# Kernel optimization log

Measured on AMD Instinct MI355X. Metric: run time of the kernel, lower is better.

The kernel has to match this reference:

```python
import jax, jax.numpy as jnp
import numpy as np

# Camera intrinsics (init kwargs of the torch module)
CAMERA_F = (248.0, 248.0)
CAMERA_C = (111.5, 111.5)
GRID_N = 41  # initial mesh = triangulated GRID_N x GRID_N grid


def _grid_faces(G):
    idx = np.arange(G * G).reshape(G, G)
    v00, v10 = idx[:-1, :-1], idx[1:, :-1]
    v01, v11 = idx[:-1, 1:], idx[1:, 1:]
    t1 = np.stack([v00, v10, v01], -1).reshape(-1, 3)
    t2 = np.stack([v10, v11, v01], -1).reshape(-1, 3)
    return np.concatenate([t1, t2], 0).astype(np.int32)


def setup_inputs() -> dict:
    key = jax.random.key(0)
    k1, k2, k3, k4 = jax.random.split(key, 4)
    verts = 0.25 * jax.random.normal(k4, (GRID_N * GRID_N, 3), jnp.float32)
    faces = jnp.asarray(_grid_faces(GRID_N))
    feat3 = jax.random.normal(k1, (256, 56, 56), jnp.float32)
    feat4 = jax.random.normal(k2, (512, 28, 28), jnp.float32)
    feat5 = jax.random.normal(k3, (512, 14, 14), jnp.float32)
    return {"feat3": feat3, "feat4": feat4, "feat5": feat5,
            "verts": verts, "faces": faces, "image_size": 224}


def _project(coords):
    # image_project: K @ [I | (0,0,0.8)] then perspective divide
    fx, fy = CAMERA_F
    cx, cy = CAMERA_C
    K = jnp.array([[fx, 0., cx], [0., fy, cy], [0., 0., 1.]], coords.dtype)
    E = jnp.array([[1., 0., 0., 0.], [0., 1., 0., 0.], [0., 0., 1., 0.8]], coords.dtype)
    P = K @ E  # [3,4]
    h = jnp.concatenate([coords, jnp.ones((coords.shape[0], 1), coords.dtype)], 1)
    pix = h @ P.T                      # [N,3]
    pix = pix / pix[:, 2:3]            # divide by s
    return pix[:, 0], pix[:, 1]


def _bilinear(x, y, feat, image_size):
    # feat: [C,H,W]; replicates original bilinear_interpolation math exactly
    dim = feat.shape[1]
    x = jnp.clip(x * dim / image_size, 0, dim - 1)
    y = jnp.clip(y * dim / image_size, 0, dim - 1)
    x1, x2 = jnp.floor(x), jnp.ceil(x)
    y1, y2 = jnp.floor(y), jnp.ceil(y)
    xi1, xi2 = x1.astype(jnp.int32), x2.astype(jnp.int32)
    yi1, yi2 = y1.astype(jnp.int32), y2.astype(jnp.int32)
    f11 = feat[:, xi1, yi1].T  # [N,C]
    f12 = feat[:, xi1, yi2].T
    f21 = feat[:, xi2, yi1].T
    f22 = feat[:, xi2, yi2].T
    w11 = ((x2 - x) * (y2 - y))[:, None]
    w12 = ((x2 - x) * (y - y1))[:, None]
    w21 = ((x - x1) * (y2 - y))[:, None]
    w22 = ((x - x1) * (y - y1))[:, None]
    return w11 * f11 + w12 * f12 + w21 * f21 + w22 * f22


def _pool(verts, feats, image_size):
    x, y = _project(verts)
    return jnp.concatenate([_bilinear(x, y, f, image_size) for f in feats], 1)


def _subdivide(vf, faces_np):
    # Vectorized equivalent of unpool_graph: one midpoint per unique
    # undirected edge, numbered by first occurrence in the per-face loop
    # order (edges (i1,i2),(i2,i3),(i3,i1) per face, faces in order).
    V = vf.shape[0]
    f = faces_np
    e = np.stack([f[:, [0, 1]], f[:, [1, 2]], f[:, [2, 0]]], 1).reshape(-1, 2)  # [3F,2]
    a, b = e.min(1), e.max(1)
    key = a.astype(np.int64) * np.int64(V) + b
    _, first_idx, inv = np.unique(key, return_index=True, return_inverse=True)
    order = np.argsort(first_idx)
    rank = np.empty(len(order), dtype=np.int64)
    rank[order] = np.arange(len(order))
    mid_idx = V + rank[inv]                       # new index per edge slot [3F]
    ue = e[np.sort(first_idx)]                    # unique edges, first-occurrence order
    mids = 0.5 * (vf[ue[:, 0]] + vf[ue[:, 1]])    # midpoint of (coords|features)
    new_vf = jnp.concatenate([vf, mids], 0)
    m = mid_idx.reshape(-1, 3)
    i1, i2, i3 = f[:, 0], f[:, 1], f[:, 2]
    i4, i5, i6 = m[:, 0], m[:, 1], m[:, 2]
    nf = np.stack([np.stack([i1, i4, i6], 1), np.stack([i2, i4, i5], 1),
                   np.stack([i3, i5, i6], 1), np.stack([i5, i4, i6], 1)], 1).reshape(-1, 3)
    return new_vf, nf.astype(np.int64)


def reference(feat3, feat4, feat5, verts, faces, image_size):
    feats = [feat3, feat4, feat5]
    faces_np = np.asarray(faces)
    # stage 1
    perc1 = _pool(verts, feats, image_size)                 # [V1,1280]
    f1 = jnp.concatenate([perc1, verts], 1)                 # [V1,1283]
    vf2, faces2 = _subdivide(jnp.concatenate([verts, f1], 1), faces_np)
    verts2, s2 = vf2[:, :3], vf2[:, 3:]
    # stage 2
    perc2 = _pool(verts2, feats, image_size)                # [V2,1280]
    f2 = jnp.concatenate([perc2, s2], 1)                    # [V2,2563]
    vf3, faces3 = _subdivide(jnp.concatenate([verts2, f2], 1), faces2)
    verts3, s3 = vf3[:, :3], vf3[:, 3:]
    # stage 3
    perc3 = _pool(verts3, feats, image_size)                # [V3,1280]
    return jnp.concatenate([perc3, s3], 1)                  # [V3,3843]
```

## Files before the change

kernel.cpp:

```cpp
#include <hip/hip_runtime.h>
#include <hip/hip_bf16.h>
#include <stdint.h>

#define NV1 1681
#define NF1 3200
#define NS1 (3*NF1)
#define NV2 6561
#define NF2 12800
#define NS2 (3*NF2)
#define NV3 25921
#define D1  1286
#define P1  1288
#define D2  2566
#define P2  2568
#define DOUT 3843
#define TSIZE 131072
#define TMASK (TSIZE-1)

__global__ __launch_bounds__(256) void transpose32(
    const float* __restrict__ in, float* __restrict__ outp, int R, int Cc)
{
  __shared__ float tile[32][33];
  int bx = blockIdx.x * 32;
  int by = blockIdx.y * 32;
  int tx = threadIdx.x, ty = threadIdx.y;
  for (int j = ty; j < 32; j += 8) {
    int r = by + j, c = bx + tx;
    if (r < R && c < Cc) tile[j][tx] = in[(size_t)r*Cc + c];
  }
  __syncthreads();
  for (int j = ty; j < 32; j += 8) {
    int orow = bx + j, oc = by + tx;
    if (orow < Cc && oc < R) outp[(size_t)orow*R + oc] = tile[tx][j];
  }
}

__global__ __launch_bounds__(320) void pool_t(
    const float* __restrict__ verts, int vstride, int nverts,
    const float* __restrict__ t3, const float* __restrict__ t4,
    const float* __restrict__ t5, float* __restrict__ out, int ostride)
{
  int v = blockIdx.x;
  if (v >= nverts) return;
  float X = verts[(size_t)v*vstride + 0];
  float Y = verts[(size_t)v*vstride + 1];
  float Z = verts[(size_t)v*vstride + 2];
  float p2 = Z + 0.8f;
  float px = (248.0f*X + 111.5f*Z + 89.2f) / p2;
  float py = (248.0f*Y + 111.5f*Z + 89.2f) / p2;

  int c4 = (int)threadIdx.x * 4;
  int m  = (c4 < 256) ? 0 : (c4 < 768) ? 1 : 2;
  int dim = (m == 0) ? 56 : (m == 1) ? 28 : 14;
  int C   = (m == 0) ? 256 : 512;
  int cb  = (m == 0) ? 0 : (m == 1) ? 256 : 768;
  const float* t = (m == 0) ? t3 : (m == 1) ? t4 : t5;

  float dimf = (float)dim;
  float x = fminf(fmaxf(px * dimf / 224.0f, 0.0f), dimf - 1.0f);
  float y = fminf(fmaxf(py * dimf / 224.0f, 0.0f), dimf - 1.0f);
  float x1 = floorf(x), x2 = ceilf(x);
  float y1 = floorf(y), y2 = ceilf(y);
  int xi1 = min(max((int)x1, 0), dim-1);
  int xi2 = min(max((int)x2, 0), dim-1);
  int yi1 = min(max((int)y1, 0), dim-1);
  int yi2 = min(max((int)y2, 0), dim-1);
  float w11 = (x2-x)*(y2-y), w12 = (x2-x)*(y-y1);
  float w21 = (x-x1)*(y2-y), w22 = (x-x1)*(y-y1);

  int cc = c4 - cb;
  const float4 f11 = *(const float4*)(t + (size_t)(xi1*dim + yi1)*C + cc);
  const float4 f12 = *(const float4*)(t + (size_t)(xi1*dim + yi2)*C + cc);
  const float4 f21 = *(const float4*)(t + (size_t)(xi2*dim + yi1)*C + cc);
  const float4 f22 = *(const float4*)(t + (size_t)(xi2*dim + yi2)*C + cc);

  float* o = out + (size_t)v*ostride + c4;
  o[0] = w11*f11.x + w12*f12.x + w21*f21.x + w22*f22.x;
  o[1] = w11*f11.y + w12*f12.y + w21*f21.y + w22*f22.y;
  o[2] = w11*f11.z + w12*f12.z + w21*f21.z + w22*f22.z;
  o[3] = w11*f11.w + w12*f12.w + w21*f21.w + w22*f22.w;
}

__global__ void copyverts1(const float* __restrict__ verts, float* __restrict__ vf1)
{
  int i = blockIdx.x*blockDim.x + threadIdx.x;
  if (i >= NV1*3) return;
  int r = i/3, c = i - 3*r;
  float v = verts[i];
  vf1[(size_t)r*P1 + c] = v;
  vf1[(size_t)r*P1 + 1283 + c] = v;
}

__global__ void edge_insert(const int* __restrict__ faces, int F, int V,
                            unsigned* __restrict__ tkey, int* __restrict__ tmin,
                            unsigned* __restrict__ keys)
{
  int s = blockIdx.x*blockDim.x + threadIdx.x;
  if (s >= 3*F) return;
  int f = s/3, k = s - 3*f;
  int a0 = faces[3*f + k];
  int a1 = faces[3*f + (k == 2 ? 0 : k+1)];
  int a = min(a0, a1), b = max(a0, a1);
  unsigned key = (unsigned)a * (unsigned)V + (unsigned)b;
  keys[s] = key;
  unsigned h = (key * 2654435761u) & TMASK;
  while (true) {
    unsigned old = atomicCAS(&tkey[h], 0xFFFFFFFFu, key);
    if (old == 0xFFFFFFFFu || old == key) { atomicMin(&tmin[h], s); break; }
    h = (h+1) & TMASK;
  }
}

__global__ void edge_first(const unsigned* __restrict__ keys, int S,
                           const unsigned* __restrict__ tkey, const int* __restrict__ tmin,
                           int* __restrict__ fslot)
{
  int s = blockIdx.x*blockDim.x + threadIdx.x;
  if (s >= S) return;
  unsigned key = keys[s];
  unsigned h = (key * 2654435761u) & TMASK;
  while (tkey[h] != key) h = (h+1) & TMASK;
  fslot[s] = tmin[h];
}

__global__ __launch_bounds__(1024) void scan_excl(const int* __restrict__ fslot,
                                                  int* __restrict__ ranks, int n)
{
  __shared__ int tmp[1024];
  int tid = (int)threadIdx.x;
  int npt = (n + 1023) >> 10;
  int base = tid * npt;
  int cnt = 0;
  for (int j = 0; j < npt; ++j) {
    int i = base + j;
    if (i < n && fslot[i] == i) cnt++;
  }
  tmp[tid] = cnt;
  __syncthreads();
  for (int off = 1; off < 1024; off <<= 1) {
    int t = (tid >= off) ? tmp[tid - off] : 0;
    __syncthreads();
    tmp[tid] += t;
    __syncthreads();
  }
  int run = tmp[tid] - cnt;
  for (int j = 0; j < npt; ++j) {
    int i = base + j;
    if (i < n) { ranks[i] = run; if (fslot[i] == i) run++; }
  }
}

__global__ void edge_mid(const unsigned* __restrict__ keys, const int* __restrict__ fslot,
                         const int* __restrict__ ranks, int S, int V,
                         int* __restrict__ mid, int* __restrict__ uea, int* __restrict__ ueb)
{
  int s = blockIdx.x*blockDim.x + threadIdx.x;
  if (s >= S) return;
  int fs = fslot[s];
  int r = ranks[fs];
  mid[s] = V + r;
  if (fs == s) {
    unsigned key = keys[s];
    uea[r] = (int)(key / (unsigned)V);
    ueb[r] = (int)(key % (unsigned)V);
  }
}

__global__ void new_faces(const int* __restrict__ faces, int F,
                          const int* __restrict__ mid, int* __restrict__ nf)
{
  int f = blockIdx.x*blockDim.x + threadIdx.x;
  if (f >= F) return;
  int i1 = faces[3*f], i2 = faces[3*f+1], i3 = faces[3*f+2];
  int i4 = mid[3*f], i5 = mid[3*f+1], i6 = mid[3*f+2];
  int* o = nf + 12*f;
  o[0]=i1; o[1]=i4; o[2]=i6;
  o[3]=i2; o[4]=i4; o[5]=i5;
  o[6]=i3; o[7]=i5; o[8]=i6;
  o[9]=i5; o[10]=i4; o[11]=i6;
}

__global__ __launch_bounds__(256) void subdivide4(
    const float* __restrict__ src, int P, int D, int Vold,
    const int* __restrict__ uea, const int* __restrict__ ueb,
    float* __restrict__ dstV, int dvs, float* __restrict__ dstS, int dss)
{
  int c4 = (blockIdx.x*256 + (int)threadIdx.x) * 4;
  int r = blockIdx.y;
  if (c4 >= D) return;
  float4 val;
  if (r < Vold) {
    val = *(const float4*)(src + (size_t)r*P + c4);
  } else {
    int e = r - Vold;
    int a = uea[e], b = ueb[e];
    float4 va = *(const float4*)(src + (size_t)a*P + c4);
    float4 vb = *(const float4*)(src + (size_t)b*P + c4);
    val.x = 0.5f*(va.x+vb.x); val.y = 0.5f*(va.y+vb.y);
    val.z = 0.5f*(va.z+vb.z); val.w = 0.5f*(va.w+vb.w);
  }
  float vv[4] = {val.x, val.y, val.z, val.w};
#pragma unroll
  for (int t = 0; t < 4; ++t) {
    int c = c4 + t;
    if (c < D) {
      if (c < 3) dstV[(size_t)r*dvs + c] = vv[t];
      else       dstS[(size_t)r*dss + (c-3)] = vv[t];
    }
  }
}

static inline char* bump(char*& p, size_t bytes) {
  char* r = p;
  p += (bytes + 255) & ~(size_t)255;
  return r;
}

extern "C" void kernel_launch(void* const* d_in, const int* in_sizes, int n_in,
                              void* d_out, int out_size, void* d_ws, size_t ws_size,
                              hipStream_t stream)
{
  const float* f3    = (const float*)d_in[0];
  const float* f4    = (const float*)d_in[1];
  const float* f5    = (const float*)d_in[2];
  const float* verts = (const float*)d_in[3];
  const int*   faces = (const int*)d_in[4];
  float* out = (float*)d_out;

  char* p = (char*)d_ws;
  float* t3     = (float*)bump(p, (size_t)3136*256*4);
  float* t4     = (float*)bump(p, (size_t)784*512*4);
  float* t5     = (float*)bump(p, (size_t)196*512*4);
  float* vf1    = (float*)bump(p, (size_t)NV1*P1*4);
  float* vf2    = (float*)bump(p, (size_t)NV2*P2*4);
  float* verts3 = (float*)bump(p, (size_t)NV3*3*4);
  int*   faces2 = (int*)  bump(p, (size_t)NF2*3*4);
  unsigned* key1 = (unsigned*)bump(p, (size_t)NS1*4);
  int* fslot1 = (int*)bump(p, (size_t)NS1*4);
  int* rank1  = (int*)bump(p, (size_t)NS1*4);
  int* mid1   = (int*)bump(p, (size_t)NS1*4);
  int* ue1a   = (int*)bump(p, (size_t)NS1*4);
  int* ue1b   = (int*)bump(p, (size_t)NS1*4);
  unsigned* key2 = (unsigned*)bump(p, (size_t)NS2*4);
  int* fslot2 = (int*)bump(p, (size_t)NS2*4);
  int* rank2  = (int*)bump(p, (size_t)NS2*4);
  int* mid2   = (int*)bump(p, (size_t)NS2*4);
  int* ue2a   = (int*)bump(p, (size_t)NS2*4);
  int* ue2b   = (int*)bump(p, (size_t)NS2*4);
  unsigned* tkey1 = (unsigned*)bump(p, (size_t)TSIZE*4);
  int*      tmin1 = (int*)     bump(p, (size_t)TSIZE*4);
  unsigned* tkey2 = (unsigned*)bump(p, (size_t)TSIZE*4);
  int*      tmin2 = (int*)     bump(p, (size_t)TSIZE*4);

  hipMemsetAsync(tkey1, 0xFF, (size_t)TSIZE*4, stream);
  hipMemsetAsync(tmin1, 0x7F, (size_t)TSIZE*4, stream);
  hipMemsetAsync(tkey2, 0xFF, (size_t)TSIZE*4, stream);
  hipMemsetAsync(tmin2, 0x7F, (size_t)TSIZE*4, stream);

  transpose32<<<dim3((3136+31)/32, (256+31)/32), dim3(32,8), 0, stream>>>(f3, t3, 256, 3136);
  transpose32<<<dim3(( 784+31)/32, (512+31)/32), dim3(32,8), 0, stream>>>(f4, t4, 512,  784);
  transpose32<<<dim3(( 196+31)/32, (512+31)/32), dim3(32,8), 0, stream>>>(f5, t5, 512,  196);

  copyverts1<<<(NV1*3 + 255)/256, 256, 0, stream>>>(verts, vf1);
  pool_t<<<NV1, 320, 0, stream>>>(verts, 3, NV1, t3, t4, t5, vf1 + 3, P1);

  edge_insert<<<(NS1+255)/256, 256, 0, stream>>>(faces, NF1, NV1, tkey1, tmin1, key1);
  edge_first <<<(NS1+255)/256, 256, 0, stream>>>(key1, NS1, tkey1, tmin1, fslot1);
  scan_excl  <<<1, 1024, 0, stream>>>(fslot1, rank1, NS1);
  edge_mid   <<<(NS1+255)/256, 256, 0, stream>>>(key1, fslot1, rank1, NS1, NV1, mid1, ue1a, ue1b);
  new_faces  <<<(NF1+255)/256, 256, 0, stream>>>(faces, NF1, mid1, faces2);

  subdivide4<<<dim3(2, NV2), 256, 0, stream>>>(
      vf1, P1, D1, NV1, ue1a, ue1b, vf2, P2, vf2 + 1283, P2);
  pool_t<<<NV2, 320, 0, stream>>>(vf2, P2, NV2, t3, t4, t5, vf2 + 3, P2);

  edge_insert<<<(NS2+255)/256, 256, 0, stream>>>(faces2, NF2, NV2, tkey2, tmin2, key2);
  edge_first <<<(NS2+255)/256, 256, 0, stream>>>(key2, NS2, tkey2, tmin2, fslot2);
  scan_excl  <<<1, 1024, 0, stream>>>(fslot2, rank2, NS2);
  edge_mid   <<<(NS2+255)/256, 256, 0, stream>>>(key2, fslot2, rank2, NS2, NV2, mid2, ue2a, ue2b);

  subdivide4<<<dim3(3, NV3), 256, 0, stream>>>(
      vf2, P2, D2, NV2, ue2a, ue2b, verts3, 3, out + 1280, DOUT);
  pool_t<<<NV3, 320, 0, stream>>>(verts3, 3, NV3, t3, t4, t5, out, DOUT);
}
```

Baseline: 665.6 us.

## Fuse subdivision with pooling and merge edge-connectivity kernels into one block

Merges the four edge-dedup kernels (insert, first-occurrence lookup, scan, midpoint assignment) and the face rebuild into a single 1024-thread block per stage. It also fuses each subdivide pass with the following pooling pass so new vertex coordinates come from shared memory rather than a reloaded row. Copyverts is folded into the first pool kernel and the four hash-table memsets become one. This removes many small launches and a full read-back of subdivided rows. In exchange, the hash work runs serialized in one block with repeated probe loops, and tmin now also starts at 0xFFFFFFFF, compared as unsigned.

```diff
diff --git a/kernel.cpp b/kernel.cpp
--- a/kernel.cpp
+++ b/kernel.cpp
@@ -35,21 +35,16 @@
   }
 }
 
-__global__ __launch_bounds__(320) void pool_t(
-    const float* __restrict__ verts, int vstride, int nverts,
+__device__ __forceinline__ void pool_row(
+    int tid, float X, float Y, float Z,
     const float* __restrict__ t3, const float* __restrict__ t4,
-    const float* __restrict__ t5, float* __restrict__ out, int ostride)
-{
-  int v = blockIdx.x;
-  if (v >= nverts) return;
-  float X = verts[(size_t)v*vstride + 0];
-  float Y = verts[(size_t)v*vstride + 1];
-  float Z = verts[(size_t)v*vstride + 2];
+    const float* __restrict__ t5, float* __restrict__ orow)
+{
   float p2 = Z + 0.8f;
   float px = (248.0f*X + 111.5f*Z + 89.2f) / p2;
   float py = (248.0f*Y + 111.5f*Z + 89.2f) / p2;
 
-  int c4 = (int)threadIdx.x * 4;
+  int c4 = tid * 4;
   int m  = (c4 < 256) ? 0 : (c4 < 768) ? 1 : 2;
   int dim = (m == 0) ? 56 : (m == 1) ? 28 : 14;
   int C   = (m == 0) ? 256 : 512;
@@ -74,66 +69,63 @@
   const float4 f21 = *(const float4*)(t + (size_t)(xi2*dim + yi1)*C + cc);
   const float4 f22 = *(const float4*)(t + (size_t)(xi2*dim + yi2)*C + cc);
 
-  float* o = out + (size_t)v*ostride + c4;
+  float* o = orow + c4;
   o[0] = w11*f11.x + w12*f12.x + w21*f21.x + w22*f22.x;
   o[1] = w11*f11.y + w12*f12.y + w21*f21.y + w22*f22.y;
   o[2] = w11*f11.z + w12*f12.z + w21*f21.z + w22*f22.z;
   o[3] = w11*f11.w + w12*f12.w + w21*f21.w + w22*f22.w;
 }
 
-__global__ void copyverts1(const float* __restrict__ verts, float* __restrict__ vf1)
-{
-  int i = blockIdx.x*blockDim.x + threadIdx.x;
-  if (i >= NV1*3) return;
-  int r = i/3, c = i - 3*r;
-  float v = verts[i];
-  vf1[(size_t)r*P1 + c] = v;
-  vf1[(size_t)r*P1 + 1283 + c] = v;
-}
-
-__global__ void edge_insert(const int* __restrict__ faces, int F, int V,
-                            unsigned* __restrict__ tkey, int* __restrict__ tmin,
-                            unsigned* __restrict__ keys)
-{
-  int s = blockIdx.x*blockDim.x + threadIdx.x;
-  if (s >= 3*F) return;
-  int f = s/3, k = s - 3*f;
-  int a0 = faces[3*f + k];
-  int a1 = faces[3*f + (k == 2 ? 0 : k+1)];
-  int a = min(a0, a1), b = max(a0, a1);
-  unsigned key = (unsigned)a * (unsigned)V + (unsigned)b;
-  keys[s] = key;
-  unsigned h = (key * 2654435761u) & TMASK;
-  while (true) {
-    unsigned old = atomicCAS(&tkey[h], 0xFFFFFFFFu, key);
-    if (old == 0xFFFFFFFFu || old == key) { atomicMin(&tmin[h], s); break; }
-    h = (h+1) & TMASK;
-  }
-}
-
-__global__ void edge_first(const unsigned* __restrict__ keys, int S,
-                           const unsigned* __restrict__ tkey, const int* __restrict__ tmin,
-                           int* __restrict__ fslot)
-{
-  int s = blockIdx.x*blockDim.x + threadIdx.x;
-  if (s >= S) return;
-  unsigned key = keys[s];
-  unsigned h = (key * 2654435761u) & TMASK;
-  while (tkey[h] != key) h = (h+1) & TMASK;
-  fslot[s] = tmin[h];
-}
-
-__global__ __launch_bounds__(1024) void scan_excl(const int* __restrict__ fslot,
-                                                  int* __restrict__ ranks, int n)
-{
+__global__ __launch_bounds__(320) void pool1f(
+    const float* __restrict__ verts,
+    const float* __restrict__ t3, const float* __restrict__ t4,
+    const float* __restrict__ t5, float* __restrict__ vf1)
+{
+  int v = blockIdx.x;
+  int tid = (int)threadIdx.x;
+  float X = verts[3*v+0], Y = verts[3*v+1], Z = verts[3*v+2];
+  if (tid < 3) {
+    float w = verts[3*v + tid];
+    vf1[(size_t)v*P1 + tid] = w;
+    vf1[(size_t)v*P1 + 1283 + tid] = w;
+  }
+  pool_row(tid, X, Y, Z, t3, t4, t5, vf1 + (size_t)v*P1 + 3);
+}
+
+__global__ __launch_bounds__(1024) void connectivity(
+    const int* __restrict__ faces, int F, int V,
+    unsigned* __restrict__ tkey, unsigned* __restrict__ tmin,
+    unsigned* __restrict__ keys,
+    int* __restrict__ mid, int* __restrict__ uea, int* __restrict__ ueb,
+    int* __restrict__ nf)
+{
+  int S = 3*F;
+  int tid = (int)threadIdx.x;
+  for (int s = tid; s < S; s += 1024) {
+    int f = s/3, k = s - 3*f;
+    int a0 = faces[3*f + k];
+    int a1 = faces[3*f + (k == 2 ? 0 : k+1)];
+    int a = min(a0, a1), b = max(a0, a1);
+    unsigned key = (unsigned)a * (unsigned)V + (unsigned)b;
+    keys[s] = key;
+    unsigned h = (key * 2654435761u) & TMASK;
+    while (true) {
+      unsigned old = atomicCAS(&tkey[h], 0xFFFFFFFFu, key);
+      if (old == 0xFFFFFFFFu || old == key) { atomicMin(&tmin[h], (unsigned)s); break; }
+      h = (h+1) & TMASK;
+    }
+  }
+  __syncthreads();
   __shared__ int tmp[1024];
-  int tid = (int)threadIdx.x;
-  int npt = (n + 1023) >> 10;
+  int npt = (S + 1023) >> 10;
   int base = tid * npt;
+  int end = min(base + npt, S);
   int cnt = 0;
-  for (int j = 0; j < npt; ++j) {
-    int i = base + j;
-    if (i < n && fslot[i] == i) cnt++;
+  for (int i = base; i < end; ++i) {
+    unsigned key = keys[i];
+    unsigned h = (key * 2654435761u) & TMASK;
+    while (tkey[h] != key) h = (h+1) & TMASK;
+    if ((int)tmin[h] == i) cnt++;
   }
   tmp[tid] = cnt;
   __syncthreads();
@@ -144,70 +136,80 @@
     __syncthreads();
   }
   int run = tmp[tid] - cnt;
-  for (int j = 0; j < npt; ++j) {
-    int i = base + j;
-    if (i < n) { ranks[i] = run; if (fslot[i] == i) run++; }
-  }
-}
-
-__global__ void edge_mid(const unsigned* __restrict__ keys, const int* __restrict__ fslot,
-                         const int* __restrict__ ranks, int S, int V,
-                         int* __restrict__ mid, int* __restrict__ uea, int* __restrict__ ueb)
-{
-  int s = blockIdx.x*blockDim.x + threadIdx.x;
-  if (s >= S) return;
-  int fs = fslot[s];
-  int r = ranks[fs];
-  mid[s] = V + r;
-  if (fs == s) {
-    unsigned key = keys[s];
-    uea[r] = (int)(key / (unsigned)V);
-    ueb[r] = (int)(key % (unsigned)V);
-  }
-}
-
-__global__ void new_faces(const int* __restrict__ faces, int F,
-                          const int* __restrict__ mid, int* __restrict__ nf)
-{
-  int f = blockIdx.x*blockDim.x + threadIdx.x;
-  if (f >= F) return;
-  int i1 = faces[3*f], i2 = faces[3*f+1], i3 = faces[3*f+2];
-  int i4 = mid[3*f], i5 = mid[3*f+1], i6 = mid[3*f+2];
-  int* o = nf + 12*f;
-  o[0]=i1; o[1]=i4; o[2]=i6;
-  o[3]=i2; o[4]=i4; o[5]=i5;
-  o[6]=i3; o[7]=i5; o[8]=i6;
-  o[9]=i5; o[10]=i4; o[11]=i6;
-}
-
-__global__ __launch_bounds__(256) void subdivide4(
-    const float* __restrict__ src, int P, int D, int Vold,
+  for (int i = base; i < end; ++i) {
+    unsigned key = keys[i];
+    unsigned h = (key * 2654435761u) & TMASK;
+    while (tkey[h] != key) h = (h+1) & TMASK;
+    if ((int)tmin[h] == i) {
+      uea[run] = (int)(key / (unsigned)V);
+      ueb[run] = (int)(key % (unsigned)V);
+      tmin[h] = (unsigned)run;
+      run++;
+    }
+  }
+  __syncthreads();
+  for (int i = base; i < end; ++i) {
+    unsigned key = keys[i];
+    unsigned h = (key * 2654435761u) & TMASK;
+    while (tkey[h] != key) h = (h+1) & TMASK;
+    mid[i] = V + (int)tmin[h];
+  }
+  if (nf) {
+    __syncthreads();
+    for (int f = tid; f < F; f += 1024) {
+      int i1 = faces[3*f], i2 = faces[3*f+1], i3 = faces[3*f+2];
+      int i4 = mid[3*f], i5 = mid[3*f+1], i6 = mid[3*f+2];
+      int* o = nf + 12*f;
+      o[0]=i1; o[1]=i4; o[2]=i6;
+      o[3]=i2; o[4]=i4; o[5]=i5;
+      o[6]=i3; o[7]=i5; o[8]=i6;
+      o[9]=i5; o[10]=i4; o[11]=i6;
+    }
+  }
+}
+
+__global__ __launch_bounds__(512) void subpool(
+    const float* __restrict__ src, int P, int Dsub, int Vold,
     const int* __restrict__ uea, const int* __restrict__ ueb,
-    float* __restrict__ dstV, int dvs, float* __restrict__ dstS, int dss)
-{
-  int c4 = (blockIdx.x*256 + (int)threadIdx.x) * 4;
-  int r = blockIdx.y;
-  if (c4 >= D) return;
-  float4 val;
-  if (r < Vold) {
-    val = *(const float4*)(src + (size_t)r*P + c4);
-  } else {
-    int e = r - Vold;
-    int a = uea[e], b = ueb[e];
-    float4 va = *(const float4*)(src + (size_t)a*P + c4);
-    float4 vb = *(const float4*)(src + (size_t)b*P + c4);
-    val.x = 0.5f*(va.x+vb.x); val.y = 0.5f*(va.y+vb.y);
-    val.z = 0.5f*(va.z+vb.z); val.w = 0.5f*(va.w+vb.w);
-  }
-  float vv[4] = {val.x, val.y, val.z, val.w};
+    const float* __restrict__ t3, const float* __restrict__ t4,
+    const float* __restrict__ t5,
+    float* __restrict__ dstV, int dvs,
+    float* __restrict__ dstS, int dss,
+    float* __restrict__ dstP, int dps)
+{
+  __shared__ float sv[3];
+  int r = blockIdx.x;
+  int tid = (int)threadIdx.x;
+  bool isCopy = (r < Vold);
+  int a = 0, b = 0;
+  if (!isCopy) { int e = r - Vold; a = uea[e]; b = ueb[e]; }
+  for (int c4 = 4*tid; c4 < Dsub; c4 += 4*512) {
+    float4 val;
+    if (isCopy) {
+      val = *(const float4*)(src + (size_t)r*P + c4);
+    } else {
+      float4 va = *(const float4*)(src + (size_t)a*P + c4);
+      float4 vb = *(const float4*)(src + (size_t)b*P + c4);
+      val.x = 0.5f*(va.x+vb.x); val.y = 0.5f*(va.y+vb.y);
+      val.z = 0.5f*(va.z+vb.z); val.w = 0.5f*(va.w+vb.w);
+    }
+    float vv[4] = {val.x, val.y, val.z, val.w};
 #pragma unroll
-  for (int t = 0; t < 4; ++t) {
-    int c = c4 + t;
-    if (c < D) {
-      if (c < 3) dstV[(size_t)r*dvs + c] = vv[t];
-      else       dstS[(size_t)r*dss + (c-3)] = vv[t];
-    }
-  }
+    for (int t = 0; t < 4; ++t) {
+      int c = c4 + t;
+      if (c >= Dsub) break;
+      float x = vv[t];
+      if (c < 3) {
+        sv[c] = x;
+        if (dstV) dstV[(size_t)r*dvs + c] = x;
+      } else {
+        dstS[(size_t)r*dss + (c-3)] = x;
+      }
+    }
+  }
+  __syncthreads();
+  if (tid < 320)
+    pool_row(tid, sv[0], sv[1], sv[2], t3, t4, t5, dstP + (size_t)r*dps);
 }
 
 static inline char* bump(char*& p, size_t bytes) {
@@ -233,53 +235,36 @@
   float* t5     = (float*)bump(p, (size_t)196*512*4);
   float* vf1    = (float*)bump(p, (size_t)NV1*P1*4);
   float* vf2    = (float*)bump(p, (size_t)NV2*P2*4);
-  float* verts3 = (float*)bump(p, (size_t)NV3*3*4);
   int*   faces2 = (int*)  bump(p, (size_t)NF2*3*4);
   unsigned* key1 = (unsigned*)bump(p, (size_t)NS1*4);
-  int* fslot1 = (int*)bump(p, (size_t)NS1*4);
-  int* rank1  = (int*)bump(p, (size_t)NS1*4);
   int* mid1   = (int*)bump(p, (size_t)NS1*4);
   int* ue1a   = (int*)bump(p, (size_t)NS1*4);
   int* ue1b   = (int*)bump(p, (size_t)NS1*4);
   unsigned* key2 = (unsigned*)bump(p, (size_t)NS2*4);
-  int* fslot2 = (int*)bump(p, (size_t)NS2*4);
-  int* rank2  = (int*)bump(p, (size_t)NS2*4);
   int* mid2   = (int*)bump(p, (size_t)NS2*4);
   int* ue2a   = (int*)bump(p, (size_t)NS2*4);
   int* ue2b   = (int*)bump(p, (size_t)NS2*4);
-  unsigned* tkey1 = (unsigned*)bump(p, (size_t)TSIZE*4);
-  int*      tmin1 = (int*)     bump(p, (size_t)TSIZE*4);
-  unsigned* tkey2 = (unsigned*)bump(p, (size_t)TSIZE*4);
-  int*      tmin2 = (int*)     bump(p, (size_t)TSIZE*4);
-
-  hipMemsetAsync(tkey1, 0xFF, (size_t)TSIZE*4, stream);
-  hipMemsetAsync(tmin1, 0x7F, (size_t)TSIZE*4, stream);
-  hipMemsetAsync(tkey2, 0xFF, (size_t)TSIZE*4, stream);
-  hipMemsetAsync(tmin2, 0x7F, (size_t)TSIZE*4, stream);
+  unsigned* tables = (unsigned*)bump(p, (size_t)4*TSIZE*4);
+  unsigned* tkey1 = tables;
+  unsigned* tmin1 = tables + TSIZE;
+  unsigned* tkey2 = tables + 2*TSIZE;
+  unsigned* tmin2 = tables + 3*TSIZE;
+
+  hipMemsetAsync(tables, 0xFF, (size_t)4*TSIZE*4, stream);
 
   transpose32<<<dim3((3136+31)/32, (256+31)/32), dim3(32,8), 0, stream>>>(f3, t3, 256, 3136);
   transpose32<<<dim3(( 784+31)/32, (512+31)/32), dim3(32,8), 0, stream>>>(f4, t4, 512,  784);
   transpose32<<<dim3(( 196+31)/32, (512+31)/32), dim3(32,8), 0, stream>>>(f5, t5, 512,  196);
 
-  copyverts1<<<(NV1*3 + 255)/256, 256, 0, stream>>>(verts, vf1);
-  pool_t<<<NV1, 320, 0, stream>>>(verts, 3, NV1, t3, t4, t5, vf1 + 3, P1);
-
-  edge_insert<<<(NS1+255)/256, 256, 0, stream>>>(faces, NF1, NV1, tkey1, tmin1, key1);
-  edge_first <<<(NS1+255)/256, 256, 0, stream>>>(key1, NS1, tkey1, tmin1, fslot1);
-  scan_excl  <<<1, 1024, 0, stream>>>(fslot1, rank1, NS1);
-  edge_mid   <<<(NS1+255)/256, 256, 0, stream>>>(key1, fslot1, rank1, NS1, NV1, mid1, ue1a, ue1b);
-  new_faces  <<<(NF1+255)/256, 256, 0, stream>>>(faces, NF1, mid1, faces2);
-
-  subdivide4<<<dim3(2, NV2), 256, 0, stream>>>(
-      vf1, P1, D1, NV1, ue1a, ue1b, vf2, P2, vf2 + 1283, P2);
-  pool_t<<<NV2, 320, 0, stream>>>(vf2, P2, NV2, t3, t4, t5, vf2 + 3, P2);
-
-  edge_insert<<<(NS2+255)/256, 256, 0, stream>>>(faces2, NF2, NV2, tkey2, tmin2, key2);
-  edge_first <<<(NS2+255)/256, 256, 0, stream>>>(key2, NS2, tkey2, tmin2, fslot2);
-  scan_excl  <<<1, 1024, 0, stream>>>(fslot2, rank2, NS2);
-  edge_mid   <<<(NS2+255)/256, 256, 0, stream>>>(key2, fslot2, rank2, NS2, NV2, mid2, ue2a, ue2b);
-
-  subdivide4<<<dim3(3, NV3), 256, 0, stream>>>(
-      vf2, P2, D2, NV2, ue2a, ue2b, verts3, 3, out + 1280, DOUT);
-  pool_t<<<NV3, 320, 0, stream>>>(verts3, 3, NV3, t3, t4, t5, out, DOUT);
-}
+  pool1f<<<NV1, 320, 0, stream>>>(verts, t3, t4, t5, vf1);
+  connectivity<<<1, 1024, 0, stream>>>(faces, NF1, NV1, tkey1, tmin1,
+                                       key1, mid1, ue1a, ue1b, faces2);
+
+  subpool<<<NV2, 512, 0, stream>>>(vf1, P1, D1, NV1, ue1a, ue1b, t3, t4, t5,
+                                   vf2, P2, vf2 + 1283, P2, vf2 + 3, P2);
+  connectivity<<<1, 1024, 0, stream>>>(faces2, NF2, NV2, tkey2, tmin2,
+                                       key2, mid2, ue2a, ue2b, nullptr);
+
+  subpool<<<NV3, 512, 0, stream>>>(vf2, P2, D2, NV2, ue2a, ue2b, t3, t4, t5,
+                                   nullptr, 0, out + 1280, DOUT, out, DOUT);
+}
```

Measured after the change: 1.069 ms. +60.6%, slower.
